# Optimization experiments

Hardware: AMD Instinct MI355X
Metric: run time of the kernel (lower is better)

Reference implementation:

```python
import jax, jax.numpy as jnp
import numpy as np

B, S, H = 1, 2048, 1024          # batch, seq_len, hidden_dim
E, I = 16, 512                    # num_experts, moe_intermediate_size
TOP_K = 4
NORM_TOPK_PROB = True


def setup_inputs() -> dict:
    key = jax.random.key(0)
    k0, k1, k2, k3, k4 = jax.random.split(key, 5)
    scale = 0.02
    return {
        "hidden_states": jax.random.normal(k0, (B, S, H), jnp.float32),
        "w_gate": jax.random.normal(k1, (H, E), jnp.float32) * scale,
        "w_gate_proj": jax.random.normal(k2, (E, H, I), jnp.float32) * scale,
        "w_up_proj": jax.random.normal(k3, (E, H, I), jnp.float32) * scale,
        "w_down_proj": jax.random.normal(k4, (E, I, H), jnp.float32) * scale,
    }


def reference(hidden_states, w_gate, w_gate_proj, w_up_proj, w_down_proj):
    b, s, h = hidden_states.shape
    x = hidden_states.reshape(-1, h)                      # [T, H]
    T = x.shape[0]

    router_logits = x @ w_gate                            # [T, E]
    routing_weights = jax.nn.softmax(router_logits.astype(jnp.float32), axis=-1)
    top_w, sel = jax.lax.top_k(routing_weights, TOP_K)    # [T, K]
    if NORM_TOPK_PROB:
        top_w = top_w / top_w.sum(axis=-1, keepdims=True)
    top_w = top_w.astype(x.dtype)

    # Per-token combine weight for every expert (0 if not in top-k).
    # Mathematically identical to the sort/gather/index_add dispatch loop.
    combine = jnp.zeros((T, E), x.dtype).at[
        jnp.arange(T)[:, None], sel].set(top_w)           # [T, E]

    def expert_step(acc, inp):
        wg, wu, wd, w = inp                               # [H,I],[H,I],[I,H],[T]
        hidden = jax.nn.silu(x @ wg) * (x @ wu)           # [T, I]
        return acc + (hidden @ wd) * w[:, None], None

    out0 = jnp.zeros_like(x)
    out, _ = jax.lax.scan(
        expert_step, out0,
        (w_gate_proj, w_up_proj, w_down_proj, combine.T))
    return out.reshape(b, s, h), router_logits
```

## Files before the change

### kernel.cpp

```cpp
#include <hip/hip_runtime.h>
#include <math.h>

constexpr int TT = 2048;
constexpr int HH = 1024;
constexpr int EE = 16;
constexpr int II = 512;

typedef unsigned short u16;
typedef short s16x8 __attribute__((ext_vector_type(8)));
typedef float f32x4 __attribute__((ext_vector_type(4)));

__device__ __forceinline__ u16 f2bf(float f) {
  unsigned u = __float_as_uint(f);
  u = (u + 0x7fffu + ((u >> 16) & 1u)) >> 16;
  return (u16)u;
}
__device__ __forceinline__ float bf2f(u16 b) {
  return __uint_as_float(((unsigned)b) << 16);
}

__device__ __forceinline__ void gl2lds16(const void* g, void* l) {
  __builtin_amdgcn_global_load_lds(
      (const __attribute__((address_space(1))) unsigned*)g,
      (__attribute__((address_space(3))) unsigned*)l, 16, 0, 0);
}

__global__ __launch_bounds__(256) void prep_kernel(
    const float* __restrict__ wgp, const float* __restrict__ wup,
    const float* __restrict__ wdp, u16* __restrict__ wgt,
    u16* __restrict__ wut, u16* __restrict__ wdt,
    int* __restrict__ counts) {
  int bid = blockIdx.x;
  int tid = threadIdx.x;
  if (bid == 0 && tid < 16) counts[tid * 16] = 0;
  int z = bid >> 8, lb = bid & 255;
  int e = z & 15, t = z >> 4;
  const float* src; u16* dst; int K, N;
  if (t == 0)      { src = wgp + (size_t)e * HH * II; dst = wgt + (size_t)e * II * HH; K = HH; N = II; }
  else if (t == 1) { src = wup + (size_t)e * HH * II; dst = wut + (size_t)e * II * HH; K = HH; N = II; }
  else             { src = wdp + (size_t)e * II * HH; dst = wdt + (size_t)e * HH * II; K = II; N = HH; }
  int nTiles = N >> 6;
  int n0 = (lb % nTiles) * 64;
  int k0 = (lb / nTiles) * 32;
  int l = tid & 63, w = tid >> 6;
  int n  = n0 + w * 16 + (l >> 2);
  int kc = l & 3;
  float v[8];
#pragma unroll
  for (int j = 0; j < 8; ++j)
    v[j] = src[(size_t)(k0 + kc * 8 + j) * N + n];
  uint4 st;
  st.x = (unsigned)f2bf(v[0]) | ((unsigned)f2bf(v[1]) << 16);
  st.y = (unsigned)f2bf(v[2]) | ((unsigned)f2bf(v[3]) << 16);
  st.z = (unsigned)f2bf(v[4]) | ((unsigned)f2bf(v[5]) << 16);
  st.w = (unsigned)f2bf(v[6]) | ((unsigned)f2bf(v[7]) << 16);
  *reinterpret_cast<uint4*>(&dst[(size_t)n * K + k0 + kc * 8]) = st;
}

__global__ __launch_bounds__(256) void router_kernel(
    const float* __restrict__ x, u16* __restrict__ xb,
    const float* __restrict__ wg, float* __restrict__ rl,
    int* __restrict__ counts, int* __restrict__ tlist,
    float* __restrict__ wlist, int* __restrict__ rowof) {
  int lane = threadIdx.x & 63, wv = threadIdx.x >> 6;
  int t = blockIdx.x * 4 + wv;
  const float* xr = x + (size_t)t * HH;
  float lg[16];
#pragma unroll
  for (int e = 0; e < 16; ++e) lg[e] = 0.f;
#pragma unroll
  for (int p = 0; p < 4; ++p) {
    int c0 = p * 256 + lane * 4;
    float4 xv = *reinterpret_cast<const float4*>(xr + c0);
    float xs4[4] = {xv.x, xv.y, xv.z, xv.w};
#pragma unroll
    for (int j = 0; j < 4; ++j) {
      const float4* wr = reinterpret_cast<const float4*>(wg + (size_t)(c0 + j) * EE);
      float4 w0 = wr[0], w1 = wr[1], w2 = wr[2], w3 = wr[3];
      float xs = xs4[j];
      lg[0]  += xs * w0.x; lg[1]  += xs * w0.y; lg[2]  += xs * w0.z; lg[3]  += xs * w0.w;
      lg[4]  += xs * w1.x; lg[5]  += xs * w1.y; lg[6]  += xs * w1.z; lg[7]  += xs * w1.w;
      lg[8]  += xs * w2.x; lg[9]  += xs * w2.y; lg[10] += xs * w2.z; lg[11] += xs * w2.w;
      lg[12] += xs * w3.x; lg[13] += xs * w3.y; lg[14] += xs * w3.z; lg[15] += xs * w3.w;
    }
    ushort4 o;
    o.x = f2bf(xv.x); o.y = f2bf(xv.y); o.z = f2bf(xv.z); o.w = f2bf(xv.w);
    *reinterpret_cast<ushort4*>(&xb[(size_t)t * HH + c0]) = o;
  }
#pragma unroll
  for (int e = 0; e < 16; ++e) {
    float p = lg[e];
#pragma unroll
    for (int s = 32; s > 0; s >>= 1) p += __shfl_xor(p, s, 64);
    lg[e] = p;
  }
  if (lane < 16) rl[(size_t)t * 16 + lane] = lg[lane];
  unsigned mask = 0;
  int sel[4]; float bl[4];
#pragma unroll
  for (int k = 0; k < 4; ++k) {
    float best = -3.4e38f; int bi = 0;
#pragma unroll
    for (int e = 0; e < 16; ++e) {
      bool ok = !((mask >> e) & 1u) && (lg[e] > best);
      best = ok ? lg[e] : best;
      bi = ok ? e : bi;
    }
    mask |= 1u << bi;
    sel[k] = bi; bl[k] = best;
  }
  float mx = bl[0];
  float wk[4]; float s = 0.f;
#pragma unroll
  for (int k = 0; k < 4; ++k) { wk[k] = expf(bl[k] - mx); s += wk[k]; }
  float inv = 1.f / s;
  if (lane < 4) {
    int k = lane;
    int e = sel[k];
    int pos = atomicAdd(&counts[e * 16], 1);
    tlist[e * TT + pos] = t;
    wlist[e * TT + pos] = wk[k] * inv;
    rowof[t * 4 + k] = e * TT + pos;
  }
}

__global__ __launch_bounds__(256, 2) void gateup_kernel(
    const u16* __restrict__ xb, const u16* __restrict__ wgt, const u16* __restrict__ wut,
    const int* __restrict__ counts,
    const int* __restrict__ tlist, const float* __restrict__ wlist,
    u16* __restrict__ hidden) {
  int bid = blockIdx.x;
  int lid = (bid & 7) * 256 + (bid >> 3);
  int e = lid >> 7, mt = (lid >> 3) & 15, nt = lid & 7;
  int cnt = counts[e * 16];
  if (mt * 128 >= cnt) return;
  __shared__ u16 As[128 * 64];
  __shared__ u16 Bg[64 * 64];
  __shared__ u16 Bu[64 * 64];
  int tid = threadIdx.x, lane = tid & 63, wv = tid >> 6;
  int wm = wv >> 1, wn = wv & 1;
  int srow = lane >> 3;
  int scol = (((lane & 7) ^ srow)) * 8;
  const u16* wgE = wgt + (size_t)e * II * HH;
  const u16* wuE = wut + (size_t)e * II * HH;
  const u16* gp[8];
#pragma unroll
  for (int c = 0; c < 8; ++c) {
    int chunk = c * 4 + wv;
    const u16* p;
    if (chunk < 16) {
      int mi = mt * 128 + chunk * 8 + srow; if (mi >= cnt) mi = cnt - 1;
      int tok = tlist[e * TT + mi];
      p = xb + (size_t)tok * HH + scol;
    } else if (chunk < 24) {
      int n = nt * 64 + (chunk - 16) * 8 + srow;
      p = wgE + (size_t)n * HH + scol;
    } else {
      int n = nt * 64 + (chunk - 24) * 8 + srow;
      p = wuE + (size_t)n * HH + scol;
    }
    gp[c] = p;
  }
  f32x4 accG[4][2] = {}; f32x4 accU[4][2] = {};
  int quad = lane >> 4, colc = lane & 15;
  for (int k0 = 0; k0 < HH; k0 += 64) {
#pragma unroll
    for (int c = 0; c < 8; ++c) {
      int chunk = c * 4 + wv;
      u16* dst = (chunk < 16) ? &As[chunk * 512]
               : (chunk < 24) ? &Bg[(chunk - 16) * 512]
                              : &Bu[(chunk - 24) * 512];
      gl2lds16(gp[c] + k0, dst);
    }
    __syncthreads();
#pragma unroll
    for (int kk = 0; kk < 64; kk += 32) {
      int gl = (kk >> 3) + quad;
      s16x8 a[4], bg[2], bu[2];
#pragma unroll
      for (int f = 0; f < 4; ++f) {
        int m = wm * 64 + f * 16 + colc;
        a[f] = *reinterpret_cast<const s16x8*>(&As[m * 64 + ((gl ^ (m & 7)) << 3)]);
      }
#pragma unroll
      for (int f = 0; f < 2; ++f) {
        int n = wn * 32 + f * 16 + colc;
        bg[f] = *reinterpret_cast<const s16x8*>(&Bg[n * 64 + ((gl ^ (n & 7)) << 3)]);
        bu[f] = *reinterpret_cast<const s16x8*>(&Bu[n * 64 + ((gl ^ (n & 7)) << 3)]);
      }
#pragma unroll
      for (int fm = 0; fm < 4; ++fm)
#pragma unroll
        for (int fn = 0; fn < 2; ++fn) {
          accG[fm][fn] = __builtin_amdgcn_mfma_f32_16x16x32_bf16(a[fm], bg[fn], accG[fm][fn], 0, 0, 0);
          accU[fm][fn] = __builtin_amdgcn_mfma_f32_16x16x32_bf16(a[fm], bu[fn], accU[fm][fn], 0, 0, 0);
        }
    }
    __syncthreads();
  }
  int hb = e * TT;
#pragma unroll
  for (int fm = 0; fm < 4; ++fm) {
#pragma unroll
    for (int r = 0; r < 4; ++r) {
      int mi = mt * 128 + wm * 64 + fm * 16 + quad * 4 + r;
      if (mi < cnt) {
        float wr = wlist[e * TT + mi];
        u16* hrow = hidden + (size_t)(hb + mi) * II + nt * 64 + wn * 32;
#pragma unroll
        for (int fn = 0; fn < 2; ++fn) {
          float g = accG[fm][fn][r], u = accU[fm][fn][r];
          float hval = wr * u * g / (1.f + expf(-g));
          hrow[fn * 16 + colc] = f2bf(hval);
        }
      }
    }
  }
}

__global__ __launch_bounds__(256, 2) void down_kernel(
    const u16* __restrict__ hidden, const u16* __restrict__ wdt,
    const int* __restrict__ counts,
    u16* __restrict__ dtmp) {
  int bid = blockIdx.x;
  int lid = (bid & 7) * 256 + (bid >> 3);
  int e = lid >> 7, mt = (lid >> 3) & 15, nt = lid & 7;
  int cnt = counts[e * 16];
  if (mt * 128 >= cnt) return;
  int hb = e * TT;
  __shared__ u16 As[128 * 64];
  __shared__ u16 Bs[128 * 64];
  int tid = threadIdx.x, lane = tid & 63, wv = tid >> 6;
  int wm = wv >> 1, wn = wv & 1;
  int srow = lane >> 3;
  int scol = (((lane & 7) ^ srow)) * 8;
  const u16* wdE = wdt + (size_t)e * HH * II;
  const u16* gA[4]; const u16* gB[4];
#pragma unroll
  for (int c = 0; c < 4; ++c) {
    int chunk = c * 4 + wv;
    int row = hb + mt * 128 + chunk * 8 + srow;
    gA[c] = hidden + (size_t)row * II + scol;
    int n = nt * 128 + chunk * 8 + srow;
    gB[c] = wdE + (size_t)n * II + scol;
  }
  f32x4 acc[4][4] = {};
  int quad = lane >> 4, colc = lane & 15;
  for (int k0 = 0; k0 < II; k0 += 64) {
#pragma unroll
    for (int c = 0; c < 4; ++c) {
      int chunk = c * 4 + wv;
      gl2lds16(gA[c] + k0, &As[chunk * 512]);
      gl2lds16(gB[c] + k0, &Bs[chunk * 512]);
    }
    __syncthreads();
#pragma unroll
    for (int kk = 0; kk < 64; kk += 32) {
      int gl = (kk >> 3) + quad;
      s16x8 a[4], b[4];
#pragma unroll
      for (int f = 0; f < 4; ++f) {
        int m = wm * 64 + f * 16 + colc;
        int n = wn * 64 + f * 16 + colc;
        a[f] = *reinterpret_cast<const s16x8*>(&As[m * 64 + ((gl ^ (m & 7)) << 3)]);
        b[f] = *reinterpret_cast<const s16x8*>(&Bs[n * 64 + ((gl ^ (n & 7)) << 3)]);
      }
#pragma unroll
      for (int fm = 0; fm < 4; ++fm)
#pragma unroll
        for (int fn = 0; fn < 4; ++fn)
          acc[fm][fn] = __builtin_amdgcn_mfma_f32_16x16x32_bf16(a[fm], b[fn], acc[fm][fn], 0, 0, 0);
    }
    __syncthreads();
  }
#pragma unroll
  for (int fm = 0; fm < 4; ++fm) {
#pragma unroll
    for (int r = 0; r < 4; ++r) {
      int mi = mt * 128 + wm * 64 + fm * 16 + quad * 4 + r;
      if (mi < cnt) {
        u16* drow = dtmp + (size_t)(hb + mi) * HH + nt * 128 + wn * 64;
#pragma unroll
        for (int fn = 0; fn < 4; ++fn)
          drow[fn * 16 + colc] = f2bf(acc[fm][fn][r]);
      }
    }
  }
}

__global__ void combine_kernel(const u16* __restrict__ dtmp, const int* __restrict__ rowof,
                               float* __restrict__ out) {
  int t = blockIdx.x, tid = threadIdx.x;
  int4 rw = reinterpret_cast<const int4*>(rowof)[t];
  int h = tid * 4;
  float s0 = 0.f, s1 = 0.f, s2 = 0.f, s3 = 0.f;
  int rows[4] = {rw.x, rw.y, rw.z, rw.w};
#pragma unroll
  for (int k = 0; k < 4; ++k) {
    ushort4 v = *reinterpret_cast<const ushort4*>(&dtmp[(size_t)rows[k] * HH + h]);
    s0 += bf2f(v.x); s1 += bf2f(v.y); s2 += bf2f(v.z); s3 += bf2f(v.w);
  }
  *reinterpret_cast<float4*>(&out[(size_t)t * HH + h]) = make_float4(s0, s1, s2, s3);
}

extern "C" void kernel_launch(void* const* d_in, const int* in_sizes, int n_in,
                              void* d_out, int out_size, void* d_ws, size_t ws_size,
                              hipStream_t stream) {
  const float* x   = (const float*)d_in[0];
  const float* wg  = (const float*)d_in[1];
  const float* wgp = (const float*)d_in[2];
  const float* wup = (const float*)d_in[3];
  const float* wdp = (const float*)d_in[4];
  float* out = (float*)d_out;
  float* rl  = out + (size_t)TT * HH;

  constexpr size_t MB = 1048576;
  char* w = (char*)d_ws;
  int*      counts  = (int*)(w + 0);
  int*      rowof   = (int*)(w + 4096);
  int*      tlist   = (int*)(w + 65536);
  float*    wlist   = (float*)(w + 65536 + 131072);
  u16*      xb      = (u16*)(w + 1 * MB);
  u16*      wgt     = (u16*)(w + 8 * MB);
  u16*      wut     = (u16*)(w + 24 * MB);
  u16*      wdt     = (u16*)(w + 40 * MB);
  u16*      hidden  = (u16*)(w + 56 * MB);
  u16*      dtmp    = (u16*)(w + 96 * MB);

  hipLaunchKernelGGL(prep_kernel, dim3(12288), dim3(256), 0, stream,
                     wgp, wup, wdp, wgt, wut, wdt, counts);
  hipLaunchKernelGGL(router_kernel, dim3(512), dim3(256), 0, stream,
                     x, xb, wg, rl, counts, tlist, wlist, rowof);
  hipLaunchKernelGGL(gateup_kernel, dim3(2048), dim3(256), 0, stream,
                     xb, wgt, wut, counts, tlist, wlist, hidden);
  hipLaunchKernelGGL(down_kernel, dim3(2048), dim3(256), 0, stream,
                     hidden, wdt, counts, dtmp);
  hipLaunchKernelGGL(combine_kernel, dim3(TT), dim3(256), 0, stream,
                     dtmp, rowof, out);
}
```

Baseline: 221.3 us.

## Fuse router into weight-prep kernel and transpose weights through LDS tiles

Merges the router and weight-conversion kernels into one launch: the first 512 blocks do routing and the remaining blocks transpose and convert expert weights to bf16. The transpose now stages a 128x64 fp32 tile in padded shared memory, so global reads are coalesced float4 loads instead of strided scalar loads. The counts array is zeroed with a memset rather than inside the kernel. This removes one launch and the uncoalesced weight reads, at the cost of shared memory per block and a mixed-role grid.

```diff
diff --git a/kernel.cpp b/kernel.cpp
--- a/kernel.cpp
+++ b/kernel.cpp
@@ -29,98 +29,110 @@
     const float* __restrict__ wgp, const float* __restrict__ wup,
     const float* __restrict__ wdp, u16* __restrict__ wgt,
     u16* __restrict__ wut, u16* __restrict__ wdt,
-    int* __restrict__ counts) {
-  int bid = blockIdx.x;
-  int tid = threadIdx.x;
-  if (bid == 0 && tid < 16) counts[tid * 16] = 0;
-  int z = bid >> 8, lb = bid & 255;
-  int e = z & 15, t = z >> 4;
-  const float* src; u16* dst; int K, N;
-  if (t == 0)      { src = wgp + (size_t)e * HH * II; dst = wgt + (size_t)e * II * HH; K = HH; N = II; }
-  else if (t == 1) { src = wup + (size_t)e * HH * II; dst = wut + (size_t)e * II * HH; K = HH; N = II; }
-  else             { src = wdp + (size_t)e * II * HH; dst = wdt + (size_t)e * HH * II; K = II; N = HH; }
-  int nTiles = N >> 6;
-  int n0 = (lb % nTiles) * 64;
-  int k0 = (lb / nTiles) * 32;
-  int l = tid & 63, w = tid >> 6;
-  int n  = n0 + w * 16 + (l >> 2);
-  int kc = l & 3;
-  float v[8];
-#pragma unroll
-  for (int j = 0; j < 8; ++j)
-    v[j] = src[(size_t)(k0 + kc * 8 + j) * N + n];
-  uint4 st;
-  st.x = (unsigned)f2bf(v[0]) | ((unsigned)f2bf(v[1]) << 16);
-  st.y = (unsigned)f2bf(v[2]) | ((unsigned)f2bf(v[3]) << 16);
-  st.z = (unsigned)f2bf(v[4]) | ((unsigned)f2bf(v[5]) << 16);
-  st.w = (unsigned)f2bf(v[6]) | ((unsigned)f2bf(v[7]) << 16);
-  *reinterpret_cast<uint4*>(&dst[(size_t)n * K + k0 + kc * 8]) = st;
-}
-
-__global__ __launch_bounds__(256) void router_kernel(
     const float* __restrict__ x, u16* __restrict__ xb,
     const float* __restrict__ wg, float* __restrict__ rl,
     int* __restrict__ counts, int* __restrict__ tlist,
     float* __restrict__ wlist, int* __restrict__ rowof) {
-  int lane = threadIdx.x & 63, wv = threadIdx.x >> 6;
-  int t = blockIdx.x * 4 + wv;
-  const float* xr = x + (size_t)t * HH;
-  float lg[16];
-#pragma unroll
-  for (int e = 0; e < 16; ++e) lg[e] = 0.f;
-#pragma unroll
-  for (int p = 0; p < 4; ++p) {
-    int c0 = p * 256 + lane * 4;
-    float4 xv = *reinterpret_cast<const float4*>(xr + c0);
-    float xs4[4] = {xv.x, xv.y, xv.z, xv.w};
-#pragma unroll
-    for (int j = 0; j < 4; ++j) {
-      const float4* wr = reinterpret_cast<const float4*>(wg + (size_t)(c0 + j) * EE);
-      float4 w0 = wr[0], w1 = wr[1], w2 = wr[2], w3 = wr[3];
-      float xs = xs4[j];
-      lg[0]  += xs * w0.x; lg[1]  += xs * w0.y; lg[2]  += xs * w0.z; lg[3]  += xs * w0.w;
-      lg[4]  += xs * w1.x; lg[5]  += xs * w1.y; lg[6]  += xs * w1.z; lg[7]  += xs * w1.w;
-      lg[8]  += xs * w2.x; lg[9]  += xs * w2.y; lg[10] += xs * w2.z; lg[11] += xs * w2.w;
-      lg[12] += xs * w3.x; lg[13] += xs * w3.y; lg[14] += xs * w3.z; lg[15] += xs * w3.w;
-    }
-    ushort4 o;
-    o.x = f2bf(xv.x); o.y = f2bf(xv.y); o.z = f2bf(xv.z); o.w = f2bf(xv.w);
-    *reinterpret_cast<ushort4*>(&xb[(size_t)t * HH + c0]) = o;
-  }
-#pragma unroll
-  for (int e = 0; e < 16; ++e) {
-    float p = lg[e];
-#pragma unroll
-    for (int s = 32; s > 0; s >>= 1) p += __shfl_xor(p, s, 64);
-    lg[e] = p;
-  }
-  if (lane < 16) rl[(size_t)t * 16 + lane] = lg[lane];
-  unsigned mask = 0;
-  int sel[4]; float bl[4];
-#pragma unroll
-  for (int k = 0; k < 4; ++k) {
-    float best = -3.4e38f; int bi = 0;
+  __shared__ float lds[128][65];
+  int bid = blockIdx.x;
+  int tid = threadIdx.x;
+  if (bid < 512) {
+    int lane = tid & 63, wv = tid >> 6;
+    int t = bid * 4 + wv;
+    const float* xr = x + (size_t)t * HH;
+    float lg[16];
+#pragma unroll
+    for (int e = 0; e < 16; ++e) lg[e] = 0.f;
+#pragma unroll
+    for (int p = 0; p < 4; ++p) {
+      int c0 = p * 256 + lane * 4;
+      float4 xv = *reinterpret_cast<const float4*>(xr + c0);
+      float xs4[4] = {xv.x, xv.y, xv.z, xv.w};
+#pragma unroll
+      for (int j = 0; j < 4; ++j) {
+        const float4* wr = reinterpret_cast<const float4*>(wg + (size_t)(c0 + j) * EE);
+        float4 w0 = wr[0], w1 = wr[1], w2 = wr[2], w3 = wr[3];
+        float xs = xs4[j];
+        lg[0]  += xs * w0.x; lg[1]  += xs * w0.y; lg[2]  += xs * w0.z; lg[3]  += xs * w0.w;
+        lg[4]  += xs * w1.x; lg[5]  += xs * w1.y; lg[6]  += xs * w1.z; lg[7]  += xs * w1.w;
+        lg[8]  += xs * w2.x; lg[9]  += xs * w2.y; lg[10] += xs * w2.z; lg[11] += xs * w2.w;
+        lg[12] += xs * w3.x; lg[13] += xs * w3.y; lg[14] += xs * w3.z; lg[15] += xs * w3.w;
+      }
+      ushort4 o;
+      o.x = f2bf(xv.x); o.y = f2bf(xv.y); o.z = f2bf(xv.z); o.w = f2bf(xv.w);
+      *reinterpret_cast<ushort4*>(&xb[(size_t)t * HH + c0]) = o;
+    }
 #pragma unroll
     for (int e = 0; e < 16; ++e) {
-      bool ok = !((mask >> e) & 1u) && (lg[e] > best);
-      best = ok ? lg[e] : best;
-      bi = ok ? e : bi;
-    }
-    mask |= 1u << bi;
-    sel[k] = bi; bl[k] = best;
-  }
-  float mx = bl[0];
-  float wk[4]; float s = 0.f;
-#pragma unroll
-  for (int k = 0; k < 4; ++k) { wk[k] = expf(bl[k] - mx); s += wk[k]; }
-  float inv = 1.f / s;
-  if (lane < 4) {
-    int k = lane;
-    int e = sel[k];
-    int pos = atomicAdd(&counts[e * 16], 1);
-    tlist[e * TT + pos] = t;
-    wlist[e * TT + pos] = wk[k] * inv;
-    rowof[t * 4 + k] = e * TT + pos;
+      float p = lg[e];
+#pragma unroll
+      for (int s = 32; s > 0; s >>= 1) p += __shfl_xor(p, s, 64);
+      lg[e] = p;
+    }
+    if (lane < 16) rl[(size_t)t * 16 + lane] = lg[lane];
+    unsigned mask = 0;
+    int sel[4]; float bl[4];
+#pragma unroll
+    for (int k = 0; k < 4; ++k) {
+      float best = -3.4e38f; int bi = 0;
+#pragma unroll
+      for (int e = 0; e < 16; ++e) {
+        bool ok = !((mask >> e) & 1u) && (lg[e] > best);
+        best = ok ? lg[e] : best;
+        bi = ok ? e : bi;
+      }
+      mask |= 1u << bi;
+      sel[k] = bi; bl[k] = best;
+    }
+    float mx = bl[0];
+    float wk[4]; float s = 0.f;
+#pragma unroll
+    for (int k = 0; k < 4; ++k) { wk[k] = expf(bl[k] - mx); s += wk[k]; }
+    float inv = 1.f / s;
+    if (lane < 4) {
+      int k = lane;
+      int e = sel[k];
+      int pos = atomicAdd(&counts[e * 16], 1);
+      tlist[e * TT + pos] = t;
+      wlist[e * TT + pos] = wk[k] * inv;
+      rowof[t * 4 + k] = e * TT + pos;
+    }
+  } else {
+    int b = bid - 512;
+    int z = b >> 6, lt = b & 63;
+    int e = z & 15, t = z >> 4;
+    const float* src; u16* dst; int K, N;
+    if (t == 0)      { src = wgp + (size_t)e * HH * II; dst = wgt + (size_t)e * II * HH; K = HH; N = II; }
+    else if (t == 1) { src = wup + (size_t)e * HH * II; dst = wut + (size_t)e * II * HH; K = HH; N = II; }
+    else             { src = wdp + (size_t)e * II * HH; dst = wdt + (size_t)e * HH * II; K = II; N = HH; }
+    int nTiles = N >> 6;
+    int n0 = (lt % nTiles) * 64;
+    int k0 = (lt / nTiles) * 128;
+    int rr = tid >> 4;
+    int cc = (tid & 15) * 4;
+#pragma unroll
+    for (int p = 0; p < 8; ++p) {
+      int r = p * 16 + rr;
+      float4 v = *reinterpret_cast<const float4*>(&src[(size_t)(k0 + r) * N + n0 + cc]);
+      lds[r][cc + 0] = v.x; lds[r][cc + 1] = v.y;
+      lds[r][cc + 2] = v.z; lds[r][cc + 3] = v.w;
+    }
+    __syncthreads();
+    int kc = tid & 15;
+    int nr = tid >> 4;
+#pragma unroll
+    for (int q = 0; q < 4; ++q) {
+      int n = q * 16 + nr;
+      float v[8];
+#pragma unroll
+      for (int j = 0; j < 8; ++j) v[j] = lds[kc * 8 + j][n];
+      uint4 st;
+      st.x = (unsigned)f2bf(v[0]) | ((unsigned)f2bf(v[1]) << 16);
+      st.y = (unsigned)f2bf(v[2]) | ((unsigned)f2bf(v[3]) << 16);
+      st.z = (unsigned)f2bf(v[4]) | ((unsigned)f2bf(v[5]) << 16);
+      st.w = (unsigned)f2bf(v[6]) | ((unsigned)f2bf(v[7]) << 16);
+      *reinterpret_cast<uint4*>(&dst[(size_t)(n0 + n) * K + k0 + kc * 8]) = st;
+    }
   }
 }
 
@@ -327,10 +339,10 @@
   u16*      hidden  = (u16*)(w + 56 * MB);
   u16*      dtmp    = (u16*)(w + 96 * MB);
 
-  hipLaunchKernelGGL(prep_kernel, dim3(12288), dim3(256), 0, stream,
-                     wgp, wup, wdp, wgt, wut, wdt, counts);
-  hipLaunchKernelGGL(router_kernel, dim3(512), dim3(256), 0, stream,
-                     x, xb, wg, rl, counts, tlist, wlist, rowof);
+  hipMemsetAsync(counts, 0, 1024, stream);
+  hipLaunchKernelGGL(prep_kernel, dim3(512 + 3072), dim3(256), 0, stream,
+                     wgp, wup, wdp, wgt, wut, wdt, x, xb, wg, rl,
+                     counts, tlist, wlist, rowof);
   hipLaunchKernelGGL(gateup_kernel, dim3(2048), dim3(256), 0, stream,
                      xb, wgt, wut, counts, tlist, wlist, hidden);
   hipLaunchKernelGGL(down_kernel, dim3(2048), dim3(256), 0, stream,
```

Measured after the change: 216.7 us. 2.0% less time.
